# Performance work log

Measured on AMD Instinct MI355X. Metric: run time of the kernel, lower is better.

Reference implementation:

```python
import jax, jax.numpy as jnp
import numpy as np


def setup_inputs() -> dict:
    key = jax.random.key(0)
    k1, k2, k3 = jax.random.split(key, 3)
    N, E, D_IN, D_OUT = 100000, 3200000, 256, 256
    x = jax.random.normal(k1, (N, D_IN), dtype=jnp.float32)
    W = jax.random.normal(k2, (D_OUT, D_IN), dtype=jnp.float32) * (1.0 / np.sqrt(D_IN))
    edge_index = jax.random.randint(k3, (2, E), 0, N, dtype=jnp.int32)
    return {"x": x, "W": W, "edge_index": edge_index}


def reference(x, W, edge_index):
    N = x.shape[0]
    # add self loops (static shape: E + N edges)
    loops = jnp.arange(N, dtype=edge_index.dtype)
    src = jnp.concatenate([edge_index[0], loops])  # [E+N]
    dst = jnp.concatenate([edge_index[1], loops])  # [E+N]
    # symmetric degree normalization: deg = bincount over source index
    deg = jax.ops.segment_sum(jnp.ones_like(src, dtype=x.dtype), src, num_segments=N)
    deg_rsqrt = jax.lax.rsqrt(deg)
    vals = deg_rsqrt[src] * deg_rsqrt[dst]  # [E+N]
    # dense projection then SpMM: out[i] = sum_e A[src_e=i] * h[dst_e]
    h = x @ W.T  # [N, D_OUT]
    msgs = vals[:, None] * h[dst]  # gather + scale
    out = jax.ops.segment_sum(msgs, src, num_segments=N)  # scatter-add
    return out
```

## Files before the change

kernel.cpp:

```cpp
#include <hip/hip_runtime.h>
#include <hip/hip_bf16.h>
#include <stdint.h>

#define D 256
#define NBUCK 391
#define BSHIFT 8
#define TILE 4096
#define CAPSH 14
#define STAGECAP 8704

typedef short short8 __attribute__((ext_vector_type(8)));
typedef float f32x4 __attribute__((ext_vector_type(4)));

__device__ __forceinline__ float bf2f(unsigned short u) {
  return __uint_as_float(((unsigned)u) << 16);
}
__device__ __forceinline__ unsigned short f2bf(float f) {
  unsigned u = __float_as_uint(f);
  unsigned r = u + 0x7FFFu + ((u >> 16) & 1u);
  return (unsigned short)(r >> 16);
}

__global__ void init_kernel(int* __restrict__ gcursor) {
  int i = blockIdx.x * 256 + threadIdx.x;
  if (i < NBUCK) gcursor[i] = i << CAPSH;
}

__launch_bounds__(256)
__global__ void binscatter_kernel(const int* __restrict__ src, const int* __restrict__ dst,
                                  int* __restrict__ gcursor, int* __restrict__ ebuf, int E) {
  __shared__ int hist[NBUCK];
  __shared__ int lstart[512];
  __shared__ int gbase[NBUCK];
  __shared__ int sc[2][512];
  __shared__ int stag[TILE];
  __shared__ unsigned short sbuck[TILE];

  int tid = threadIdx.x;
  int base = blockIdx.x * TILE;
  int tilecount = E - base;
  if (tilecount > TILE) tilecount = TILE;

  for (int i = tid; i < NBUCK; i += 256) hist[i] = 0;
  __syncthreads();

  int esrc[16], edst[16];
#pragma unroll
  for (int k = 0; k < 16; k++) {
    int e = base + k * 256 + tid;
    if (e < E) {
      esrc[k] = src[e];
      edst[k] = dst[e];
      atomicAdd(&hist[esrc[k] >> BSHIFT], 1);
    } else {
      esrc[k] = -1;
      edst[k] = 0;
    }
  }
  __syncthreads();

  for (int i = tid; i < 512; i += 256) sc[0][i] = (i < NBUCK) ? hist[i] : 0;
  __syncthreads();
  int d = 0;
  for (int off = 1; off < 512; off <<= 1) {
    for (int i = tid; i < 512; i += 256) {
      int v = sc[d][i];
      if (i >= off) v += sc[d][i - off];
      sc[d ^ 1][i] = v;
    }
    __syncthreads();
    d ^= 1;
  }
  for (int i = tid; i < 512; i += 256) lstart[i] = (i == 0) ? 0 : sc[d][i - 1];
  __syncthreads();

  for (int b = tid; b < NBUCK; b += 256) {
    int c = hist[b];
    if (c) gbase[b] = atomicAdd(&gcursor[b], c);
  }
  __syncthreads();

  for (int i = tid; i < NBUCK; i += 256) hist[i] = 0;
  __syncthreads();

#pragma unroll
  for (int k = 0; k < 16; k++) {
    if (esrc[k] >= 0) {
      int b = esrc[k] >> BSHIFT;
      int r = atomicAdd(&hist[b], 1);
      int pos = lstart[b] + r;
      stag[pos] = edst[k] | ((esrc[k] & 255) << 20);
      sbuck[pos] = (unsigned short)b;
    }
  }
  __syncthreads();

  for (int s = tid; s < tilecount; s += 256) {
    int b = sbuck[s];
    int pos = gbase[b] + (s - lstart[b]);
    if (pos < ((b + 1) << CAPSH))
      ebuf[pos] = stag[s];
  }
}

__launch_bounds__(256)
__global__ void bucketsort_kernel(const int* __restrict__ ebuf, const int* __restrict__ gcursor,
                                  int* __restrict__ csr,
                                  int2* __restrict__ meta, float* __restrict__ rnorm, int N) {
  __shared__ int seg[STAGECAP];
  __shared__ int ncnt[256];
  __shared__ int nstart[256];
  __shared__ int sc[2][256];
  int tid = threadIdx.x;
  int b = blockIdx.x;
  int base = b << CAPSH;
  int cnt = gcursor[b] - base;
  int node0 = b << BSHIFT;

  int lim = (cnt < STAGECAP) ? cnt : STAGECAP;
  for (int s = tid; s < lim; s += 256) seg[s] = ebuf[base + s];
  ncnt[tid] = 0;
  __syncthreads();

  for (int s = tid; s < cnt; s += 256) {
    int v = (s < STAGECAP) ? seg[s] : ebuf[base + s];
    atomicAdd(&ncnt[v >> 20], 1);
  }
  __syncthreads();

  int mycnt = ncnt[tid];
  sc[0][tid] = mycnt;
  __syncthreads();
  int d = 0;
  for (int off = 1; off < 256; off <<= 1) {
    int v = sc[d][tid];
    if (tid >= off) v += sc[d][tid - off];
    sc[d ^ 1][tid] = v;
    __syncthreads();
    d ^= 1;
  }
  nstart[tid] = (tid == 0) ? 0 : sc[d][tid - 1];
  __syncthreads();

  int node = node0 + tid;
  if (node < N) {
    meta[node] = make_int2(base + nstart[tid], mycnt);
    rnorm[node] = rsqrtf((float)(mycnt + 1));
  }

  ncnt[tid] = 0;
  __syncthreads();
  for (int s = tid; s < cnt; s += 256) {
    int v = (s < STAGECAP) ? seg[s] : ebuf[base + s];
    int nl = v >> 20;
    int r = atomicAdd(&ncnt[nl], 1);
    csr[base + nstart[nl] + r] = v & 0xFFFFF;
  }
}

__global__ void convw_kernel(const float* __restrict__ w, unsigned short* __restrict__ wb) {
  int i4 = blockIdx.x * 256 + threadIdx.x;
  int elem = i4 * 4;
  const float4 v = *(const float4*)&w[elem];
  ushort4 o;
  o.x = f2bf(v.x); o.y = f2bf(v.y); o.z = f2bf(v.z); o.w = f2bf(v.w);
  *(ushort4*)&wb[elem] = o;
}

__launch_bounds__(256)
__global__ void gemm_kernel(const float* __restrict__ X,
                            const unsigned short* __restrict__ B,
                            unsigned short* __restrict__ Hout,
                            const float* __restrict__ rnorm, int n) {
  __shared__ unsigned short sA[128 * 32];
  __shared__ unsigned short sB[128 * 32];
  int tid = threadIdx.x;
  int wave = tid >> 6, lane = tid & 63;
  int wm = wave >> 1, wn = wave & 1;
  int l16 = lane & 15, quad = lane >> 4;
  int arow0 = blockIdx.x * 128;
  int brow0 = blockIdx.y * 128;

  f32x4 acc[4][4];
  const f32x4 zero = {0.f, 0.f, 0.f, 0.f};
#pragma unroll
  for (int i = 0; i < 4; i++)
#pragma unroll
    for (int j = 0; j < 4; j++) acc[i][j] = zero;

  for (int k0 = 0; k0 < 256; k0 += 32) {
#pragma unroll
    for (int it = 0; it < 2; ++it) {
      int c = it * 256 + tid;
      int row = c >> 2, cc = (c & 3) * 8;
      int grow = arow0 + row;
      ushort4 lo = make_ushort4(0, 0, 0, 0), hi = make_ushort4(0, 0, 0, 0);
      if (grow < n) {
        const float4 v0 = *(const float4*)&X[(size_t)grow * 256 + k0 + cc];
        const float4 v1 = *(const float4*)&X[(size_t)grow * 256 + k0 + cc + 4];
        lo.x = f2bf(v0.x); lo.y = f2bf(v0.y); lo.z = f2bf(v0.z); lo.w = f2bf(v0.w);
        hi.x = f2bf(v1.x); hi.y = f2bf(v1.y); hi.z = f2bf(v1.z); hi.w = f2bf(v1.w);
      }
      *(ushort4*)&sA[c * 8] = lo;
      *(ushort4*)&sA[c * 8 + 4] = hi;
      *(int4*)&sB[c * 8] = *(const int4*)&B[(brow0 + row) * 256 + k0 + cc];
    }
    __syncthreads();
    short8 af[4], bfr[4];
#pragma unroll
    for (int i = 0; i < 4; i++)
      af[i] = *(const short8*)&sA[(wm * 64 + i * 16 + l16) * 32 + quad * 8];
#pragma unroll
    for (int j = 0; j < 4; j++)
      bfr[j] = *(const short8*)&sB[(wn * 64 + j * 16 + l16) * 32 + quad * 8];
#pragma unroll
    for (int i = 0; i < 4; i++)
#pragma unroll
      for (int j = 0; j < 4; j++)
        acc[i][j] = __builtin_amdgcn_mfma_f32_16x16x32_bf16(af[i], bfr[j], acc[i][j], 0, 0, 0);
    __syncthreads();
  }

#pragma unroll
  for (int i = 0; i < 4; i++) {
    int rowb = arow0 + wm * 64 + i * 16 + quad * 4;
#pragma unroll
    for (int r = 0; r < 4; r++) {
      int gr = rowb + r;
      float rn = (gr < n) ? rnorm[gr] : 0.f;
#pragma unroll
      for (int j = 0; j < 4; j++) {
        int col = brow0 + wn * 64 + j * 16 + l16;
        Hout[(size_t)gr * 256 + col] = f2bf(acc[i][j][r] * rn);
      }
    }
  }
}

__launch_bounds__(256)
__global__ void gather_kernel(const unsigned short* __restrict__ hs,
                              const int2* __restrict__ meta,
                              const float* __restrict__ rnorm,
                              const int* __restrict__ csr,
                              float* __restrict__ out, int n) {
  int wave = threadIdx.x >> 6, lane = threadIdx.x & 63;
  int colbase = (blockIdx.x & 1) * 128;
  int node = (blockIdx.x >> 1) * 4 + wave;
  if (node >= n) return;
  long long mm = *(const long long*)&meta[node];
  int start = (int)mm, cnt = (int)(mm >> 32);
  const unsigned short* hcol = hs + colbase + lane * 2;
  float a0 = 0.f, a1 = 0.f;
  for (int base = 0; base < cnt; base += 64) {
    int m = cnt - base;
    if (m > 64) m = 64;
    int idxv = 0;
    if (lane < m) idxv = csr[start + base + lane];
    int t = 0;
    for (; t + 8 <= m; t += 8) {
      int d0 = __shfl(idxv, t);
      int d1 = __shfl(idxv, t + 1);
      int d2 = __shfl(idxv, t + 2);
      int d3 = __shfl(idxv, t + 3);
      int d4 = __shfl(idxv, t + 4);
      int d5 = __shfl(idxv, t + 5);
      int d6 = __shfl(idxv, t + 6);
      int d7 = __shfl(idxv, t + 7);
      unsigned u0 = *(const unsigned*)&hcol[d0 * 256];
      unsigned u1 = *(const unsigned*)&hcol[d1 * 256];
      unsigned u2 = *(const unsigned*)&hcol[d2 * 256];
      unsigned u3 = *(const unsigned*)&hcol[d3 * 256];
      unsigned u4 = *(const unsigned*)&hcol[d4 * 256];
      unsigned u5 = *(const unsigned*)&hcol[d5 * 256];
      unsigned u6 = *(const unsigned*)&hcol[d6 * 256];
      unsigned u7 = *(const unsigned*)&hcol[d7 * 256];
      a0 += bf2f((unsigned short)u0) + bf2f((unsigned short)u1) +
            bf2f((unsigned short)u2) + bf2f((unsigned short)u3) +
            bf2f((unsigned short)u4) + bf2f((unsigned short)u5) +
            bf2f((unsigned short)u6) + bf2f((unsigned short)u7);
      a1 += bf2f((unsigned short)(u0 >> 16)) + bf2f((unsigned short)(u1 >> 16)) +
            bf2f((unsigned short)(u2 >> 16)) + bf2f((unsigned short)(u3 >> 16)) +
            bf2f((unsigned short)(u4 >> 16)) + bf2f((unsigned short)(u5 >> 16)) +
            bf2f((unsigned short)(u6 >> 16)) + bf2f((unsigned short)(u7 >> 16));
    }
    for (; t < m; ++t) {
      int dd = __shfl(idxv, t);
      unsigned u = *(const unsigned*)&hcol[dd * 256];
      a0 += bf2f((unsigned short)u);
      a1 += bf2f((unsigned short)(u >> 16));
    }
  }
  unsigned us = *(const unsigned*)&hcol[node * 256];
  float rn = rnorm[node];
  float2 o;
  o.x = rn * (a0 + bf2f((unsigned short)us));
  o.y = rn * (a1 + bf2f((unsigned short)(us >> 16)));
  *(float2*)&out[(size_t)node * 256 + colbase + lane * 2] = o;
}

extern "C" void kernel_launch(void* const* d_in, const int* in_sizes, int n_in,
                              void* d_out, int out_size, void* d_ws, size_t ws_size,
                              hipStream_t stream) {
  const float* x = (const float*)d_in[0];
  const float* W = (const float*)d_in[1];
  const int* ei = (const int*)d_in[2];
  float* out = (float*)d_out;

  int N = in_sizes[0] / D;
  int E = in_sizes[2] / 2;
  int NPAD = (N + 127) & ~127;
  const int* src = ei;
  const int* dst = ei + E;

  char* p = (char*)d_ws;
  auto alloc = [&](size_t b) {
    char* r = p;
    p += (b + 255) & ~(size_t)255;
    return r;
  };
  unsigned short* wb = (unsigned short*)alloc((size_t)D * D * 2);
  unsigned short* hb = (unsigned short*)alloc((size_t)NPAD * D * 2);
  int* csr = (int*)alloc((size_t)NBUCK << CAPSH << 2);
  int2* meta = (int2*)alloc((size_t)N * 8);
  float* rnorm = (float*)alloc((size_t)N * 4);
  int* gcursor = (int*)alloc(NBUCK * 4);
  int* ebuf = (int*)hb;

  init_kernel<<<2, 256, 0, stream>>>(gcursor);
  binscatter_kernel<<<(E + TILE - 1) / TILE, 256, 0, stream>>>(src, dst, gcursor, ebuf, E);
  bucketsort_kernel<<<NBUCK, 256, 0, stream>>>(ebuf, gcursor, csr, meta, rnorm, N);
  convw_kernel<<<(D * D / 4) / 256, 256, 0, stream>>>(W, wb);
  gemm_kernel<<<dim3(NPAD / 128, D / 128), 256, 0, stream>>>(x, wb, hb, rnorm, N);
  gather_kernel<<<2 * ((N + 3) / 4), 256, 0, stream>>>(hb, meta, rnorm, csr, out, N);
}
```

Baseline: 489.3 us.

## Fuse weight bf16 conversion into GEMM and remap blocks for X-tile L2 reuse

Removes the separate weight-conversion kernel: the GEMM now loads fp32 W directly and converts it to bf16 while staging it into shared memory. The grid becomes one-dimensional and is remapped so that groups of 16 consecutive blocks cover 8 row tiles times both column halves. Blocks sharing an X row tile therefore run close together, which should improve L2 reuse of X. In exchange, every block re-reads W as fp32, doubling W load bytes and adding conversion ALU work to each block.

```diff
diff --git a/kernel.cpp b/kernel.cpp
--- a/kernel.cpp
+++ b/kernel.cpp
@@ -158,28 +158,25 @@
   }
 }
 
-__global__ void convw_kernel(const float* __restrict__ w, unsigned short* __restrict__ wb) {
-  int i4 = blockIdx.x * 256 + threadIdx.x;
-  int elem = i4 * 4;
-  const float4 v = *(const float4*)&w[elem];
-  ushort4 o;
-  o.x = f2bf(v.x); o.y = f2bf(v.y); o.z = f2bf(v.z); o.w = f2bf(v.w);
-  *(ushort4*)&wb[elem] = o;
-}
-
 __launch_bounds__(256)
 __global__ void gemm_kernel(const float* __restrict__ X,
-                            const unsigned short* __restrict__ B,
+                            const float* __restrict__ W,
                             unsigned short* __restrict__ Hout,
-                            const float* __restrict__ rnorm, int n) {
+                            const float* __restrict__ rnorm, int n, int ntiles) {
   __shared__ unsigned short sA[128 * 32];
   __shared__ unsigned short sB[128 * 32];
+  int bid = blockIdx.x;
+  int group = bid >> 4, slot = bid & 15;
+  int rowtile = group * 8 + (slot & 7);
+  int ch = slot >> 3;
+  if (rowtile >= ntiles) return;
+  int arow0 = rowtile * 128;
+  int brow0 = ch * 128;
+
   int tid = threadIdx.x;
   int wave = tid >> 6, lane = tid & 63;
   int wm = wave >> 1, wn = wave & 1;
   int l16 = lane & 15, quad = lane >> 4;
-  int arow0 = blockIdx.x * 128;
-  int brow0 = blockIdx.y * 128;
 
   f32x4 acc[4][4];
   const f32x4 zero = {0.f, 0.f, 0.f, 0.f};
@@ -203,7 +200,13 @@
       }
       *(ushort4*)&sA[c * 8] = lo;
       *(ushort4*)&sA[c * 8 + 4] = hi;
-      *(int4*)&sB[c * 8] = *(const int4*)&B[(brow0 + row) * 256 + k0 + cc];
+      const float4 w0 = *(const float4*)&W[(size_t)(brow0 + row) * 256 + k0 + cc];
+      const float4 w1 = *(const float4*)&W[(size_t)(brow0 + row) * 256 + k0 + cc + 4];
+      ushort4 blo, bhi;
+      blo.x = f2bf(w0.x); blo.y = f2bf(w0.y); blo.z = f2bf(w0.z); blo.w = f2bf(w0.w);
+      bhi.x = f2bf(w1.x); bhi.y = f2bf(w1.y); bhi.z = f2bf(w1.z); bhi.w = f2bf(w1.w);
+      *(ushort4*)&sB[c * 8] = blo;
+      *(ushort4*)&sB[c * 8 + 4] = bhi;
     }
     __syncthreads();
     short8 af[4], bfr[4];
@@ -309,6 +312,7 @@
   int N = in_sizes[0] / D;
   int E = in_sizes[2] / 2;
   int NPAD = (N + 127) & ~127;
+  int NTILES = NPAD / 128;
   const int* src = ei;
   const int* dst = ei + E;
 
@@ -318,7 +322,6 @@
     p += (b + 255) & ~(size_t)255;
     return r;
   };
-  unsigned short* wb = (unsigned short*)alloc((size_t)D * D * 2);
   unsigned short* hb = (unsigned short*)alloc((size_t)NPAD * D * 2);
   int* csr = (int*)alloc((size_t)NBUCK << CAPSH << 2);
   int2* meta = (int2*)alloc((size_t)N * 8);
@@ -329,7 +332,6 @@
   init_kernel<<<2, 256, 0, stream>>>(gcursor);
   binscatter_kernel<<<(E + TILE - 1) / TILE, 256, 0, stream>>>(src, dst, gcursor, ebuf, E);
   bucketsort_kernel<<<NBUCK, 256, 0, stream>>>(ebuf, gcursor, csr, meta, rnorm, N);
-  convw_kernel<<<(D * D / 4) / 256, 256, 0, stream>>>(W, wb);
-  gemm_kernel<<<dim3(NPAD / 128, D / 128), 256, 0, stream>>>(x, wb, hb, rnorm, N);
+  gemm_kernel<<<((NTILES + 7) / 8) * 16, 256, 0, stream>>>(x, W, hb, rnorm, N, NTILES);
   gather_kernel<<<2 * ((N + 3) / 4), 256, 0, stream>>>(hb, meta, rnorm, csr, out, N);
 }
```

Measured after the change: 496.7 us. About the same (+1.5%).
